# Performance work log

Hardware: AMD Instinct MI355X
Metric: run time of the kernel (lower is better)

Reference implementation:

```python
import jax, jax.numpy as jnp
import numpy as np

N_HEAD = 12


def setup_inputs() -> dict:
    key = jax.random.key(0)
    ks = jax.random.split(key, 5)
    B, T, C = 2, 2048, 768
    x = jax.random.normal(ks[0], (B, T, C), dtype=jnp.float32)
    w_attn = jax.random.normal(ks[1], (3 * C, C), dtype=jnp.float32) * 0.02
    b_attn = jax.random.normal(ks[2], (3 * C,), dtype=jnp.float32) * 0.02
    w_proj = jax.random.normal(ks[3], (C, C), dtype=jnp.float32) * 0.02
    b_proj = jax.random.normal(ks[4], (C,), dtype=jnp.float32) * 0.02
    return {"x": x, "w_attn": w_attn, "b_attn": b_attn, "w_proj": w_proj, "b_proj": b_proj}


def reference(x, w_attn, b_attn, w_proj, b_proj):
    B, T, C = x.shape
    H = N_HEAD
    D = C // H
    # fused QKV projection (torch Linear: x @ W.T + b)
    qkv = x @ w_attn.T + b_attn                      # [B, T, 3C]
    q, k, v = jnp.split(qkv, 3, axis=-1)
    q = q.reshape(B, T, H, D).transpose(0, 2, 1, 3)  # [B, H, T, D]
    k = k.reshape(B, T, H, D).transpose(0, 2, 1, 3)
    v = v.reshape(B, T, H, D).transpose(0, 2, 1, 3)
    # NOTE: original scales by 1/sqrt(k.size(0)) == 1/sqrt(B) (batch!), reproduced faithfully
    scale = 1.0 / jnp.sqrt(jnp.asarray(B, dtype=x.dtype))
    scores = jnp.einsum("bhtd,bhsd->bhts", q, k) * scale  # [B, H, T, T]
    causal = jnp.tril(jnp.ones((T, T), dtype=bool))
    scores = jnp.where(causal[None, None], scores, jnp.asarray(-jnp.inf, dtype=x.dtype))
    attn = jax.nn.softmax(scores, axis=-1)
    # dropout layers are identity in eval mode
    out = jnp.einsum("bhts,bhsd->bhtd", attn, v)     # [B, H, T, D]
    out = out.transpose(0, 2, 1, 3).reshape(B, T, C)
    return out @ w_proj.T + b_proj
```

## Files before the change

### kernel.cpp

```cpp
#include <hip/hip_runtime.h>
#include <hip/hip_bf16.h>
#include <stdint.h>

typedef __bf16 bf16;
typedef __bf16 bf16x4 __attribute__((ext_vector_type(4)));
typedef __bf16 bf16x8 __attribute__((ext_vector_type(8)));
typedef float f32x4 __attribute__((ext_vector_type(4)));

__device__ __forceinline__ f32x4 mfma16(bf16x8 a, bf16x8 b, f32x4 c) {
    return __builtin_amdgcn_mfma_f32_16x16x32_bf16(a, b, c, 0, 0, 0);
}

__device__ __forceinline__ void gload_lds16(const void* g, void* l) {
    __builtin_amdgcn_global_load_lds((__attribute__((address_space(1))) void*)g,
                                     (__attribute__((address_space(3))) void*)l,
                                     16, 0, 0);
}

__global__ void k_cast3(const float* __restrict__ x, const float* __restrict__ wa,
                        const float* __restrict__ wp, bf16* __restrict__ xb,
                        bf16* __restrict__ wab, bf16* __restrict__ wpb) {
    const int N1 = 786432, N2 = 442368, N3 = 147456;
    int i = blockIdx.x * blockDim.x + threadIdx.x;
    int stride = gridDim.x * blockDim.x;
    for (; i < N1 + N2 + N3; i += stride) {
        const float* src; bf16* dst; int j = i;
        if (j < N1)           { src = x;  dst = xb; }
        else if (j < N1 + N2) { src = wa; dst = wab; j -= N1; }
        else                  { src = wp; dst = wpb; j -= N1 + N2; }
        float4 v = reinterpret_cast<const float4*>(src)[j];
        bf16x4 o = { (bf16)v.x, (bf16)v.y, (bf16)v.z, (bf16)v.w };
        reinterpret_cast<bf16x4*>(dst)[j] = o;
    }
}

template<bool BF16_OUT>
__global__ __launch_bounds__(256) void k_gemm_bt(
        const bf16* __restrict__ A, const bf16* __restrict__ W,
        const float* __restrict__ bias, void* __restrict__ Cout,
        int M, int N, int K) {
    __shared__ bf16 As[128 * 64];
    __shared__ bf16 Ws[128 * 64];
    const int tid = threadIdx.x;
    const int l = tid & 63, w = tid >> 6;
    const int lr = l & 15, lq = l >> 4;
    const int wm = w >> 1, wn = w & 1;
    const int bm = blockIdx.y * 128, bn = blockIdx.x * 128;

    f32x4 acc[4][4] = {};

    for (int k0 = 0; k0 < K; k0 += 64) {
        __syncthreads();
        #pragma unroll
        for (int i = 0; i < 4; ++i) {
            int c = tid + i * 256;
            int row = c >> 3, j = c & 7;
            int src8 = (j ^ (row & 7)) * 8;
            gload_lds16(A + (size_t)(bm + row) * K + k0 + src8, As + c * 8);
            gload_lds16(W + (size_t)(bn + row) * K + k0 + src8, Ws + c * 8);
        }
        __syncthreads();
        bf16x8 af[2][4], wf[2][4];
        #pragma unroll
        for (int ks = 0; ks < 2; ++ks)
            #pragma unroll
            for (int f = 0; f < 4; ++f) {
                int ra = wm * 64 + f * 16 + lr;
                int rb = wn * 64 + f * 16 + lr;
                af[ks][f] = *reinterpret_cast<const bf16x8*>(
                    As + ra * 64 + (((ks * 4 + lq) ^ (lr & 7)) * 8));
                wf[ks][f] = *reinterpret_cast<const bf16x8*>(
                    Ws + rb * 64 + (((ks * 4 + lq) ^ (lr & 7)) * 8));
            }
        #pragma unroll
        for (int ks = 0; ks < 2; ++ks)
            #pragma unroll
            for (int fm = 0; fm < 4; ++fm)
                #pragma unroll
                for (int fn = 0; fn < 4; ++fn)
                    acc[fm][fn] = mfma16(af[ks][fm], wf[ks][fn], acc[fm][fn]);
    }

    #pragma unroll
    for (int fm = 0; fm < 4; ++fm) {
        #pragma unroll
        for (int fn = 0; fn < 4; ++fn) {
            int row = bm + wm * 64 + fm * 16 + lq * 4;
            int col = bn + wn * 64 + fn * 16 + lr;
            float bv = bias[col];
            #pragma unroll
            for (int r = 0; r < 4; ++r) {
                float v = acc[fm][fn][r] + bv;
                if (BF16_OUT)
                    ((bf16*)Cout)[(size_t)(row + r) * N + col] = (bf16)v;
                else
                    ((float*)Cout)[(size_t)(row + r) * N + col] = v;
            }
        }
    }
}

#define CLOG2E 1.02014439f

__global__ __launch_bounds__(256, 3) void k_flash_attn(
        const bf16* __restrict__ qkv, bf16* __restrict__ att,
        float* __restrict__ part, int mode) {
    __shared__ bf16 Ks[3][4096];
    __shared__ bf16 Vt[2][64][72];

    const int tid = threadIdx.x;
    const int l = tid & 63, w = tid >> 6;
    const int lr = l & 15, lq = l >> 4;

    const int bid = blockIdx.x;
    int qb, h, b, jt0, jt1, slot;
    bool dopart;
    if (mode) {
        int bh = bid % 24, idx = bid / 24;
        h = bh % 12; b = bh / 12;
        if (idx < 16)      { qb = 16 + idx;  jt0 = 0;  jt1 = 16;     dopart = true;  slot = (bh * 16 + idx) * 2; }
        else if (idx < 32) { qb = 47 - idx;  jt0 = 16; jt1 = qb + 1; dopart = true;  slot = (bh * 16 + (qb - 16)) * 2 + 1; }
        else               { qb = 47 - idx;  jt0 = 0;  jt1 = qb + 1; dopart = false; slot = 0; }
    } else {
        const int s = bid >> 8, i = (bid >> 3) & 31, t7 = bid & 7;
        if (s == 0)      qb = i;
        else if (s == 2) qb = (i + 16) & 31;
        else             qb = (i < 8) ? (31 - 2 * i) : (i < 16) ? (30 - 2 * i)
                           : (i < 24) ? (62 - 2 * i) : (63 - 2 * i);
        const int hb = s * 8 + t7;
        h = hb % 12; b = hb / 12;
        jt0 = 0; jt1 = qb + 1; dopart = false; slot = 0;
    }

    const bf16* Qp = qkv + (size_t)b * 2048 * 2304 + h * 64;
    const bf16* Kp = Qp + 768;
    const bf16* Vp = Qp + 1536;

    const int qr0 = qb * 64 + w * 16;

    bf16x8 qf[2];
    #pragma unroll
    for (int ks = 0; ks < 2; ++ks)
        qf[ks] = *reinterpret_cast<const bf16x8*>(
            Qp + (size_t)(qr0 + lr) * 2304 + ks * 32 + lq * 8);

    f32x4 o[4] = {};
    float lsum = 0.f;

    auto stageK = [&](int buf, int kv0) {
        #pragma unroll
        for (int ii = 0; ii < 2; ++ii) {
            int c = tid + ii * 256;
            int row = c >> 3, j = c & 7;
            gload_lds16(Kp + (size_t)(kv0 + row) * 2304 + ((j ^ (row & 7)) * 8),
                        &Ks[buf][c * 8]);
        }
    };
    bf16x8 vv0, vv1;
    auto loadV = [&](int kv0) {
        vv0 = *reinterpret_cast<const bf16x8*>(
            Vp + (size_t)(kv0 + (tid >> 3)) * 2304 + (tid & 7) * 8);
        vv1 = *reinterpret_cast<const bf16x8*>(
            Vp + (size_t)(kv0 + 32 + (tid >> 3)) * 2304 + (tid & 7) * 8);
    };
    auto writeV = [&](int buf) {
        int kv = tid >> 3, d0 = (tid & 7) * 8;
        int sw = (tid & 7) << 3;
        #pragma unroll
        for (int j = 0; j < 8; ++j) {
            int d = d0 + j;
            Vt[buf][d][kv ^ sw]        = vv0[j];
            Vt[buf][d][(kv + 32) ^ sw] = vv1[j];
        }
    };

    stageK(0, jt0 * 64);
    if (jt1 > jt0 + 1) stageK(1, (jt0 + 1) * 64);
    loadV(jt0 * 64);
    asm volatile("s_waitcnt vmcnt(0)" ::: "memory");
    writeV(0);
    asm volatile("s_waitcnt lgkmcnt(0)" ::: "memory");
    __builtin_amdgcn_s_barrier();
    asm volatile("" ::: "memory");

    for (int jt = jt0; jt < jt1; ++jt) {
        const int curV = (jt - jt0) & 1;
        const int curK = (jt - jt0) % 3;
        const int kv0 = jt * 64;
        if (jt + 1 < jt1) loadV(kv0 + 64);
        if (jt + 2 < jt1) stageK((jt + 2 - jt0) % 3, kv0 + 128);

        const bool diag = (jt == qb);
        const int rsw = lr & 7;
        float p[4][4];
        __builtin_amdgcn_s_setprio(1);
        #pragma unroll
        for (int t = 0; t < 4; ++t) {
            f32x4 sacc = {0.f, 0.f, 0.f, 0.f};
            #pragma unroll
            for (int ks = 0; ks < 2; ++ks) {
                bf16x8 kf = *reinterpret_cast<const bf16x8*>(
                    &Ks[curK][(t * 16 + lr) * 64 + (((ks * 4 + lq) ^ rsw) * 8)]);
                sacc = mfma16(kf, qf[ks], sacc);
            }
            #pragma unroll
            for (int r = 0; r < 4; ++r) {
                float e = __builtin_amdgcn_exp2f(sacc[r] * CLOG2E);
                if (diag && (t * 16 + lq * 4 + r > w * 16 + lr)) e = 0.f;
                p[t][r] = e;
                lsum += e;
            }
        }
        __builtin_amdgcn_s_setprio(0);

        unsigned P0[4], P1[4];
        #pragma unroll
        for (int t = 0; t < 4; ++t) {
            asm("v_cvt_pk_bf16_f32 %0, %1, %2" : "=v"(P0[t]) : "v"(p[t][0]), "v"(p[t][1]));
            asm("v_cvt_pk_bf16_f32 %0, %1, %2" : "=v"(P1[t]) : "v"(p[t][2]), "v"(p[t][3]));
        }
        __builtin_amdgcn_s_setprio(1);
        #pragma unroll
        for (int ks = 0; ks < 2; ++ks) {
            unsigned a0 = P0[2 * ks], b0 = P0[2 * ks + 1];
            asm volatile("v_permlane32_swap_b32 %0, %1" : "+v"(a0), "+v"(b0));
            asm volatile("v_permlane16_swap_b32 %0, %1" : "+v"(a0), "+v"(b0));
            unsigned a1 = P1[2 * ks], b1 = P1[2 * ks + 1];
            asm volatile("v_permlane32_swap_b32 %0, %1" : "+v"(a1), "+v"(b1));
            asm volatile("v_permlane16_swap_b32 %0, %1" : "+v"(a1), "+v"(b1));
            union { unsigned u[4]; bf16x8 v8; } pk_;
            pk_.u[0] = a0; pk_.u[1] = a1; pk_.u[2] = b0; pk_.u[3] = b1;
            bf16x8 pa = pk_.v8;
            #pragma unroll
            for (int db = 0; db < 4; ++db) {
                int row = db * 16 + lr;
                bf16x8 vf = *reinterpret_cast<const bf16x8*>(
                    &Vt[curV][row][(ks * 32 + lq * 8) ^ (((row >> 3) & 7) << 3)]);
                o[db] = mfma16(pa, vf, o[db]);
            }
        }
        __builtin_amdgcn_s_setprio(0);

        if (jt + 1 < jt1) writeV(curV ^ 1);
        asm volatile("s_waitcnt lgkmcnt(0)" ::: "memory");
        __builtin_amdgcn_s_barrier();
        asm volatile("" ::: "memory");
    }

    lsum += __shfl_xor(lsum, 16);
    lsum += __shfl_xor(lsum, 32);

    if (dopart) {
        float* pb = part + (size_t)slot * 4160;
        #pragma unroll
        for (int db = 0; db < 4; ++db)
            #pragma unroll
            for (int r = 0; r < 4; ++r)
                pb[(w * 16 + lq * 4 + r) * 64 + db * 16 + lr] = o[db][r];
        if (lq == 0) pb[4096 + w * 16 + lr] = lsum;
    } else {
        float inv[4];
        #pragma unroll
        for (int r = 0; r < 4; ++r)
            inv[r] = 1.0f / __shfl(lsum, lq * 4 + r);
        #pragma unroll
        for (int db = 0; db < 4; ++db)
            #pragma unroll
            for (int r = 0; r < 4; ++r) {
                float v = o[db][r] * inv[r];
                att[(size_t)(b * 2048 + qr0 + lq * 4 + r) * 768 + h * 64 + db * 16 + lr] = (bf16)v;
            }
    }
}

__global__ __launch_bounds__(256) void k_attn_reduce(
        const float* __restrict__ part, bf16* __restrict__ att) {
    int g = blockIdx.x;
    int bh = g / 16, q16 = g % 16, qb = 16 + q16;
    int h = bh % 12, b = bh / 12;
    const float* p0 = part + (size_t)((bh * 16 + q16) * 2) * 4160;
    const float* p1 = p0 + 4160;
    for (int e = threadIdx.x; e < 4096; e += 256) {
        int row = e >> 6, col = e & 63;
        float O = p0[e] + p1[e];
        float L = p0[4096 + row] + p1[4096 + row];
        att[(size_t)(b * 2048 + qb * 64 + row) * 768 + h * 64 + col] = (bf16)(O / L);
    }
}

extern "C" void kernel_launch(void* const* d_in, const int* in_sizes, int n_in,
                              void* d_out, int out_size, void* d_ws, size_t ws_size,
                              hipStream_t stream) {
    const float* x      = (const float*)d_in[0];
    const float* w_attn = (const float*)d_in[1];
    const float* b_attn = (const float*)d_in[2];
    const float* w_proj = (const float*)d_in[3];
    const float* b_proj = (const float*)d_in[4];

    char* ws = (char*)d_ws;
    bf16* xb   = (bf16*)(ws + 0);
    bf16* wab  = (bf16*)(ws + 6291456);
    bf16* wpb  = (bf16*)(ws + 9830400);
    bf16* qkv  = (bf16*)(ws + 11010048);
    bf16* att  = (bf16*)(ws + 29884416);
    float* part = (float*)(ws + 36175872);
    const unsigned long long WS_NEEDED = 36175872ull + 12779520ull;

    k_cast3<<<2048, 256, 0, stream>>>(x, w_attn, w_proj, xb, wab, wpb);

    dim3 g1(2304 / 128, 4096 / 128);
    k_gemm_bt<true><<<g1, 256, 0, stream>>>(xb, wab, b_attn, qkv, 4096, 2304, 768);

    if (ws_size >= WS_NEEDED) {
        k_flash_attn<<<1152, 256, 0, stream>>>(qkv, att, part, 1);
        k_attn_reduce<<<384, 256, 0, stream>>>(part, att);
    } else {
        k_flash_attn<<<768, 256, 0, stream>>>(qkv, att, part, 0);
    }

    dim3 g2(768 / 128, 4096 / 128);
    k_gemm_bt<false><<<g2, 256, 0, stream>>>(att, wpb, b_proj, d_out, 4096, 768, 768);
}
```

Before: 88.39 us.

## Shrink V tile padding, rotate V writes, raise occupancy, tree-reduce row sums

Drops the padding from the transposed V shared-memory tile (72 to 64 columns) and changes the XOR swizzle to use the row's low bits. Each thread now rotates the order of its element writes so that lanes in a group hit different LDS banks. Launch bounds go from 3 to 4 blocks per SM to reach higher occupancy. The causal mask and the probability sum are moved out of the exp loop into a separate masked pass and a tree reduction, which shortens the serial dependency chain but may increase register pressure under the tighter bound.

```diff
diff --git a/kernel.cpp b/kernel.cpp
--- a/kernel.cpp
+++ b/kernel.cpp
@@ -102,11 +102,11 @@
 
 #define CLOG2E 1.02014439f
 
-__global__ __launch_bounds__(256, 3) void k_flash_attn(
+__global__ __launch_bounds__(256, 4) void k_flash_attn(
         const bf16* __restrict__ qkv, bf16* __restrict__ att,
         float* __restrict__ part, int mode) {
     __shared__ bf16 Ks[3][4096];
-    __shared__ bf16 Vt[2][64][72];
+    __shared__ bf16 Vt[2][64][64];
 
     const int tid = threadIdx.x;
     const int l = tid & 63, w = tid >> 6;
@@ -164,13 +164,13 @@
             Vp + (size_t)(kv0 + 32 + (tid >> 3)) * 2304 + (tid & 7) * 8);
     };
     auto writeV = [&](int buf) {
-        int kv = tid >> 3, d0 = (tid & 7) * 8;
-        int sw = (tid & 7) << 3;
-        #pragma unroll
-        for (int j = 0; j < 8; ++j) {
-            int d = d0 + j;
-            Vt[buf][d][kv ^ sw]        = vv0[j];
-            Vt[buf][d][(kv + 32) ^ sw] = vv1[j];
+        int kv = tid >> 3, d0 = (tid & 7) * 8, t7v = tid & 7;
+        #pragma unroll
+        for (int jj = 0; jj < 8; ++jj) {
+            int jp = (jj + t7v) & 7;
+            int d = d0 + jp, sw = jp << 3;
+            Vt[buf][d][kv ^ sw]        = vv0[jp];
+            Vt[buf][d][(kv + 32) ^ sw] = vv1[jp];
         }
     };
 
@@ -204,14 +204,24 @@
                 sacc = mfma16(kf, qf[ks], sacc);
             }
             #pragma unroll
-            for (int r = 0; r < 4; ++r) {
-                float e = __builtin_amdgcn_exp2f(sacc[r] * CLOG2E);
-                if (diag && (t * 16 + lq * 4 + r > w * 16 + lr)) e = 0.f;
-                p[t][r] = e;
-                lsum += e;
-            }
+            for (int r = 0; r < 4; ++r)
+                p[t][r] = __builtin_amdgcn_exp2f(sacc[r] * CLOG2E);
         }
         __builtin_amdgcn_s_setprio(0);
+        if (diag) {
+            #pragma unroll
+            for (int t = 0; t < 4; ++t)
+                #pragma unroll
+                for (int r = 0; r < 4; ++r)
+                    if (t * 16 + lq * 4 + r > w * 16 + lr) p[t][r] = 0.f;
+        }
+        {
+            float s0 = (p[0][0] + p[0][1]) + (p[0][2] + p[0][3]);
+            float s1 = (p[1][0] + p[1][1]) + (p[1][2] + p[1][3]);
+            float s2 = (p[2][0] + p[2][1]) + (p[2][2] + p[2][3]);
+            float s3 = (p[3][0] + p[3][1]) + (p[3][2] + p[3][3]);
+            lsum += (s0 + s1) + (s2 + s3);
+        }
 
         unsigned P0[4], P1[4];
         #pragma unroll
@@ -235,7 +245,7 @@
             for (int db = 0; db < 4; ++db) {
                 int row = db * 16 + lr;
                 bf16x8 vf = *reinterpret_cast<const bf16x8*>(
-                    &Vt[curV][row][(ks * 32 + lq * 8) ^ (((row >> 3) & 7) << 3)]);
+                    &Vt[curV][row][(ks * 32 + lq * 8) ^ ((row & 7) << 3)]);
                 o[db] = mfma16(pa, vf, o[db]);
             }
         }
```

Result: slower. 104.0 us (+17.6%).
